# Kernel tuning notes

Hardware: AMD Instinct MI355X
Metric: run time of the kernel (lower is better)

Reference implementation:

```python
import jax, jax.numpy as jnp
import numpy as np

B, C, T = 8, 512, 2048
G = 32          # GroupNorm groups
HEADS = 8       # C // head_channels(64)
EPS = 1e-5


def setup_inputs() -> dict:
    key = jax.random.key(0)
    ks = jax.random.split(key, 7)
    s = 0.02
    return {
        "x": jax.random.normal(ks[0], (B, C, T), dtype=jnp.float32),
        "gn_w": jnp.ones((C,), dtype=jnp.float32),
        "gn_b": jnp.zeros((C,), dtype=jnp.float32),
        "qkv_w": jax.random.normal(ks[1], (3 * C, C), dtype=jnp.float32) * s,
        "qkv_b": jnp.zeros((3 * C,), dtype=jnp.float32),
        "proj_w": jax.random.normal(ks[2], (C, C), dtype=jnp.float32) * s,
        "proj_b": jnp.zeros((C,), dtype=jnp.float32),
    }


def reference(x, gn_w, gn_b, qkv_w, qkv_b, proj_w, proj_b):
    b, c, t = x.shape
    ch = c // HEADS
    # GroupNorm(32, C): normalize over (channels-in-group, T)
    xg = x.reshape(b, G, (c // G) * t)
    mu = jnp.mean(xg, axis=-1, keepdims=True)
    var = jnp.var(xg, axis=-1, keepdims=True)
    h = ((xg - mu) * jax.lax.rsqrt(var + EPS)).reshape(b, c, t)
    h = h * gn_w[:, None] + gn_b[:, None]
    # 1x1 Conv1d -> pointwise linear over channels
    qkv = jnp.einsum('oc,bct->bot', qkv_w, h) + qkv_b[:, None]  # [b, 3c, t]
    q, k, v = jnp.split(qkv, 3, axis=1)
    scale = ch ** -0.25
    q = (q * scale).reshape(b * HEADS, ch, t)
    k = (k * scale).reshape(b * HEADS, ch, t)
    v = v.reshape(b * HEADS, ch, t)
    w = jnp.einsum('bct,bcs->bts', q, k)  # [b*H, t, t]
    w = jax.nn.softmax(w.astype(jnp.float32), axis=-1).astype(q.dtype)
    a = jnp.einsum('bts,bcs->bct', w, v).reshape(b, c, t)
    out = jnp.einsum('oc,bct->bot', proj_w, a) + proj_b[:, None]
    return x + out
```

## Files before the change

kernel.cpp:

```cpp
#include <hip/hip_runtime.h>
#include <hip/hip_bf16.h>
#include <math.h>

#define NB 8
#define NC 512
#define NT 2048
#define NG 32
#define NH 8
#define CH 64

typedef __attribute__((ext_vector_type(8))) short short8;
typedef __attribute__((ext_vector_type(4))) short short4v;
typedef __attribute__((ext_vector_type(4))) float floatx4;

static __device__ __forceinline__ short f2bf(float f) {
    __hip_bfloat16 h = __float2bfloat16(f);
    return *reinterpret_cast<short*>(&h);
}

static __device__ __forceinline__ int pk2bf_trunc(float lo, float hi) {
    return (int)__builtin_amdgcn_perm(__builtin_bit_cast(unsigned, hi),
                                      __builtin_bit_cast(unsigned, lo),
                                      0x07060302u);
}

static __device__ __forceinline__ void gload_lds16(const short* g, short* l) {
    __builtin_amdgcn_global_load_lds(
        (const __attribute__((address_space(1))) void*)g,
        (__attribute__((address_space(3))) void*)l, 16, 0, 0);
}

__global__ __launch_bounds__(256) void castw_kernel(
    const float* __restrict__ w, short* __restrict__ o, int n4)
{
    const int i = blockIdx.x * 256 + threadIdx.x;
    if (i < n4) {
        float4 v = ((const float4*)w)[i];
        short4v s;
        s.x = f2bf(v.x); s.y = f2bf(v.y); s.z = f2bf(v.z); s.w = f2bf(v.w);
        *(short4v*)&o[i * 4] = s;
    }
}

__global__ __launch_bounds__(256) void gn_stats_kernel(
    const float* __restrict__ x, float* __restrict__ stats)
{
    __shared__ float red[16];
    const int tid = threadIdx.x;
    const int grp = blockIdx.x;
    const float4* xp = (const float4*)(x + (size_t)grp * 16 * NT);

    float s = 0.f, ss = 0.f;
    for (int i = tid; i < 8192; i += 256) {
        float4 v = xp[i];
        s  += v.x + v.y + v.z + v.w;
        ss += v.x*v.x + v.y*v.y + v.z*v.z + v.w*v.w;
    }
    #pragma unroll
    for (int o = 32; o > 0; o >>= 1) {
        s  += __shfl_down(s,  o, 64);
        ss += __shfl_down(ss, o, 64);
    }
    const int lane = tid & 63, wid = tid >> 6;
    if (lane == 0) { red[wid] = s; red[8 + wid] = ss; }
    __syncthreads();
    if (tid == 0) {
        const float inv = 1.f / 32768.f;
        const float mean = (red[0] + red[1] + red[2] + red[3]) * inv;
        const float var  = (red[8] + red[9] + red[10] + red[11]) * inv - mean * mean;
        stats[grp * 2]     = mean;
        stats[grp * 2 + 1] = rsqrtf(var + 1e-5f);
    }
}

__global__ __launch_bounds__(256) void gn_apply_kernel(
    const float* __restrict__ x, const float* __restrict__ gw,
    const float* __restrict__ gb, const float* __restrict__ stats,
    short* __restrict__ ht)
{
    __shared__ float wc_s[NC], bc_s[NC];
    const int tid = threadIdx.x;
    const int b = blockIdx.y;
    const int t0 = blockIdx.x * 64;

    for (int c = tid; c < NC; c += 256) {
        const int g = c >> 4;
        const float mean = stats[(b * NG + g) * 2];
        const float rstd = stats[(b * NG + g) * 2 + 1];
        const float wc = gw[c] * rstd;
        wc_s[c] = wc;
        bc_s[c] = gb[c] - mean * wc;
    }
    __syncthreads();

    const int t  = t0 + (tid >> 2);
    const int lc = tid & 3;
    const float* xb = x + (size_t)b * NC * NT + t;
    short* out = ht + ((size_t)b * NT + t) * NC;

    for (int k = 0; k < 16; ++k) {
        const int c0 = lc * 8 + k * 32;
        short8 v;
        #pragma unroll
        for (int j = 0; j < 8; ++j) {
            const int c = c0 + j;
            v[j] = f2bf(xb[(size_t)c * NT] * wc_s[c] + bc_s[c]);
        }
        *(short8*)&out[c0] = v;
    }
}

#define BK 32
__global__ __launch_bounds__(256) void qkv_gemm_kernel(
    const short* __restrict__ wb, const short* __restrict__ ht,
    const float* __restrict__ bias,
    short* __restrict__ q_t, short* __restrict__ k_t, short* __restrict__ vv)
{
    __shared__ short As[128 * BK];
    __shared__ short Bs[128 * BK];
    const int tid = threadIdx.x;
    const int wv = tid >> 6, lane = tid & 63;
    const int l16 = lane & 15, quad = lane >> 4;
    const int n0 = blockIdx.x * 128;
    const int m0 = blockIdx.y * 128;
    const int wm = wv & 1, wn = wv >> 1;

    floatx4 acc[4][4];
    #pragma unroll
    for (int i = 0; i < 4; ++i)
        #pragma unroll
        for (int j = 0; j < 4; ++j) acc[i][j] = (floatx4){0.f, 0.f, 0.f, 0.f};

    const short* gsrc = (wv < 2) ? wb : ht;
    const int rbase = (wv & 1) * 64;
    const int tile0 = (wv < 2) ? m0 : n0;
    short* lbuf = (wv < 2) ? As : Bs;
    const int lrow = lane >> 2;
    const int lcol = (lane & 3) * 8;

    for (int k0 = 0; k0 < 512; k0 += BK) {
        __syncthreads();
        #pragma unroll
        for (int ch = 0; ch < 4; ++ch) {
            const int row = rbase + ch * 16 + lrow;
            gload_lds16(gsrc + (size_t)(tile0 + row) * 512 + k0 + lcol,
                        lbuf + (rbase + ch * 16) * BK);
        }
        __syncthreads();

        short8 af[4], bfr[4];
        #pragma unroll
        for (int i = 0; i < 4; ++i) {
            af[i]  = *(const short8*)&As[(wm * 64 + i * 16 + l16) * BK + quad * 8];
            bfr[i] = *(const short8*)&Bs[(wn * 64 + i * 16 + l16) * BK + quad * 8];
        }
        #pragma unroll
        for (int i = 0; i < 4; ++i)
            #pragma unroll
            for (int j = 0; j < 4; ++j)
                acc[i][j] = __builtin_amdgcn_mfma_f32_16x16x32_bf16(
                    af[i], bfr[j], acc[i][j], 0, 0, 0);
    }

    const float kscale = 0.35355339059327373f;
    const float qscale = 0.35355339059327373f * 1.4426950408889634f;
    #pragma unroll
    for (int i = 0; i < 4; ++i) {
        const int o16 = m0 + wm * 64 + i * 16;
        const int sel = o16 >> 9;
        const int hh  = (o16 >> 6) & 7;
        const int c16 = o16 & 63;
        const float4 b4 = *(const float4*)&bias[o16 + quad * 4];
        const float sc = (sel == 0) ? qscale : kscale;
        #pragma unroll
        for (int j = 0; j < 4; ++j) {
            const int tg = n0 + wn * 64 + j * 16 + l16;
            const int b = tg >> 11, t = tg & 2047;
            floatx4 v = acc[i][j];
            v[0] += b4.x; v[1] += b4.y; v[2] += b4.z; v[3] += b4.w;
            if (sel < 2) {
                short4v s;
                s.x = f2bf(v[0] * sc); s.y = f2bf(v[1] * sc);
                s.z = f2bf(v[2] * sc); s.w = f2bf(v[3] * sc);
                short* dst = (sel == 0 ? q_t : k_t) +
                    (((size_t)(b * NH + hh) * NT + t) * CH + c16 + quad * 4);
                *(short4v*)dst = s;
            } else {
                short* dst = vv + ((size_t)(b * NH + hh) * CH + c16 + quad * 4) * NT + t;
                #pragma unroll
                for (int r = 0; r < 4; ++r) dst[(size_t)r * NT] = f2bf(v[r]);
            }
        }
    }
}

__global__ __launch_bounds__(256, 2) void attn_kernel(
    const short* __restrict__ qg, const short* __restrict__ kg,
    const short* __restrict__ vg, short* __restrict__ at)
{
    __shared__ short qps[256 * 64];
    __shared__ short kt[2][64 * 64];
    __shared__ short vs[2][64 * 64];

    const int tid = threadIdx.x;
    const int wv = tid >> 6, lane = tid & 63;
    const int l16 = lane & 15, quad = lane >> 4;
    const int xr = l16 & 7;
    const int t0 = blockIdx.x * 256;
    const int bh = blockIdx.y;
    const int b = bh >> 3, hd = bh & 7;
    const short* qh = qg + (size_t)bh * NT * CH;
    const short* kh = kg + (size_t)bh * NT * CH;
    const short* vh = vg + (size_t)bh * CH * NT;

    #pragma unroll
    for (int q = 0; q < 8; ++q) {
        const int F = (wv * 8 + q) * 64 + lane;
        const int row = F >> 3, cc = (F & 7) ^ (row & 7);
        gload_lds16(qh + (size_t)(t0 + row) * CH + cc * 8, &qps[(wv * 8 + q) * 512]);
    }
    #pragma unroll
    for (int q = 0; q < 2; ++q) {
        const int F = (wv * 2 + q) * 64 + lane;
        const int row = F >> 3, cc = (F & 7) ^ (row & 7);
        gload_lds16(kh + (size_t)row * CH + cc * 8, &kt[0][(wv * 2 + q) * 512]);
        gload_lds16(vh + (size_t)row * NT + cc * 8, &vs[0][(wv * 2 + q) * 512]);
    }
    __syncthreads();

    short8 bq[4][2];
    #pragma unroll
    for (int qt = 0; qt < 4; ++qt) {
        const int row = wv * 64 + qt * 16 + l16;
        #pragma unroll
        for (int ks = 0; ks < 2; ++ks) {
            const int c = (quad | (ks << 2)) ^ xr;
            bq[qt][ks] = *(const short8*)&qps[row * 64 + c * 8];
        }
    }

    floatx4 Oa[4][4];
    #pragma unroll
    for (int ct = 0; ct < 4; ++ct)
        #pragma unroll
        for (int qt = 0; qt < 4; ++qt) Oa[ct][qt] = (floatx4){0.f, 0.f, 0.f, 0.f};
    float l_part[4] = {0.f, 0.f, 0.f, 0.f};

    for (int it = 0; it < NT / 64; ++it) {
        __syncthreads();
        if (it + 1 < NT / 64) {
            const int s0n = (it + 1) * 64;
            short* kb = kt[(it + 1) & 1];
            short* vb = vs[(it + 1) & 1];
            #pragma unroll
            for (int q = 0; q < 2; ++q) {
                const int F = (wv * 2 + q) * 64 + lane;
                const int row = F >> 3, cc = (F & 7) ^ (row & 7);
                gload_lds16(kh + (size_t)(s0n + row) * CH + cc * 8, kb + (wv * 2 + q) * 512);
                gload_lds16(vh + (size_t)row * NT + s0n + cc * 8, vb + (wv * 2 + q) * 512);
            }
        }
        const short* kc = kt[it & 1];
        const short* vc = vs[it & 1];

        floatx4 sacc[4][4];
        #pragma unroll
        for (int nt = 0; nt < 4; ++nt)
            #pragma unroll
            for (int qt = 0; qt < 4; ++qt) sacc[nt][qt] = (floatx4){0.f, 0.f, 0.f, 0.f};
        #pragma unroll
        for (int ks = 0; ks < 2; ++ks) {
            const int c = (quad | (ks << 2)) ^ xr;
            #pragma unroll
            for (int nt = 0; nt < 4; ++nt) {
                short8 ak = *(const short8*)&kc[(nt * 16 + l16) * 64 + c * 8];
                #pragma unroll
                for (int qt = 0; qt < 4; ++qt)
                    sacc[nt][qt] = __builtin_amdgcn_mfma_f32_16x16x32_bf16(
                        ak, bq[qt][ks], sacc[nt][qt], 0, 0, 0);
            }
        }

        #pragma unroll
        for (int qt = 0; qt < 4; ++qt) {
            float sn[4];
            #pragma unroll
            for (int nt = 0; nt < 4; ++nt) {
                const float p0 = __builtin_amdgcn_exp2f(sacc[nt][qt][0]);
                const float p1 = __builtin_amdgcn_exp2f(sacc[nt][qt][1]);
                const float p2 = __builtin_amdgcn_exp2f(sacc[nt][qt][2]);
                const float p3 = __builtin_amdgcn_exp2f(sacc[nt][qt][3]);
                sacc[nt][qt][0] = p0; sacc[nt][qt][1] = p1;
                sacc[nt][qt][2] = p2; sacc[nt][qt][3] = p3;
                sn[nt] = (p0 + p1) + (p2 + p3);
            }
            l_part[qt] += (sn[0] + sn[1]) + (sn[2] + sn[3]);
        }

        #pragma unroll
        for (int qt = 0; qt < 4; ++qt) {
            const int row = wv * 64 + qt * 16 + l16;
            #pragma unroll
            for (int nt = 0; nt < 4; ++nt) {
                const int cw = (2 * nt + (quad >> 1)) ^ xr;
                int2 pv;
                pv.x = pk2bf_trunc(sacc[nt][qt][0], sacc[nt][qt][1]);
                pv.y = pk2bf_trunc(sacc[nt][qt][2], sacc[nt][qt][3]);
                *(int2*)&qps[row * 64 + cw * 8 + (quad & 1) * 4] = pv;
            }
        }

        #pragma unroll
        for (int ks = 0; ks < 2; ++ks) {
            const int c = (quad | (ks << 2)) ^ xr;
            short8 bp[4];
            #pragma unroll
            for (int qt = 0; qt < 4; ++qt)
                bp[qt] = *(const short8*)&qps[(wv * 64 + qt * 16 + l16) * 64 + c * 8];
            #pragma unroll
            for (int ct = 0; ct < 4; ++ct) {
                short8 av = *(const short8*)&vc[(ct * 16 + l16) * 64 + c * 8];
                #pragma unroll
                for (int qt = 0; qt < 4; ++qt)
                    Oa[ct][qt] = __builtin_amdgcn_mfma_f32_16x16x32_bf16(
                        av, bp[qt], Oa[ct][qt], 0, 0, 0);
            }
        }
    }

    #pragma unroll
    for (int qt = 0; qt < 4; ++qt) {
        float l = l_part[qt];
        l += __shfl_xor(l, 16, 64);
        l += __shfl_xor(l, 32, 64);
        const float rl = 1.f / l;
        const int t = t0 + wv * 64 + qt * 16 + l16;
        short* dst = at + ((size_t)b * NT + t) * NC + hd * CH;
        #pragma unroll
        for (int ct = 0; ct < 4; ++ct) {
            int2 s;
            s.x = pk2bf_trunc(Oa[ct][qt][0] * rl, Oa[ct][qt][1] * rl);
            s.y = pk2bf_trunc(Oa[ct][qt][2] * rl, Oa[ct][qt][3] * rl);
            *(int2*)&dst[ct * 16 + quad * 4] = s;
        }
    }
}

__global__ __launch_bounds__(256) void proj_gemm_kernel(
    const short* __restrict__ wb, const short* __restrict__ at,
    const float* __restrict__ bias, const float* __restrict__ xres,
    float* __restrict__ out)
{
    __shared__ short As[128 * BK];
    __shared__ short Bs[128 * BK];
    const int tid = threadIdx.x;
    const int wv = tid >> 6, lane = tid & 63;
    const int l16 = lane & 15, quad = lane >> 4;
    const int n0 = blockIdx.x * 128;
    const int m0 = blockIdx.y * 128;
    const int wm = wv & 1, wn = wv >> 1;

    floatx4 acc[4][4];
    #pragma unroll
    for (int i = 0; i < 4; ++i)
        #pragma unroll
        for (int j = 0; j < 4; ++j) acc[i][j] = (floatx4){0.f, 0.f, 0.f, 0.f};

    const short* gsrc = (wv < 2) ? wb : at;
    const int rbase = (wv & 1) * 64;
    const int tile0 = (wv < 2) ? m0 : n0;
    short* lbuf = (wv < 2) ? As : Bs;
    const int lrow = lane >> 2;
    const int lcol = (lane & 3) * 8;

    for (int k0 = 0; k0 < 512; k0 += BK) {
        __syncthreads();
        #pragma unroll
        for (int ch = 0; ch < 4; ++ch) {
            const int row = rbase + ch * 16 + lrow;
            gload_lds16(gsrc + (size_t)(tile0 + row) * 512 + k0 + lcol,
                        lbuf + (rbase + ch * 16) * BK);
        }
        __syncthreads();

        short8 af[4], bfr[4];
        #pragma unroll
        for (int i = 0; i < 4; ++i) {
            af[i]  = *(const short8*)&As[(wm * 64 + i * 16 + l16) * BK + quad * 8];
            bfr[i] = *(const short8*)&Bs[(wn * 64 + i * 16 + l16) * BK + quad * 8];
        }
        #pragma unroll
        for (int i = 0; i < 4; ++i)
            #pragma unroll
            for (int j = 0; j < 4; ++j)
                acc[i][j] = __builtin_amdgcn_mfma_f32_16x16x32_bf16(
                    af[i], bfr[j], acc[i][j], 0, 0, 0);
    }

    #pragma unroll
    for (int i = 0; i < 4; ++i) {
        const int o16 = m0 + wm * 64 + i * 16;
        const float4 b4 = *(const float4*)&bias[o16 + quad * 4];
        #pragma unroll
        for (int j = 0; j < 4; ++j) {
            const int tg = n0 + wn * 64 + j * 16 + l16;
            const int b = tg >> 11, t = tg & 2047;
            const size_t base = ((size_t)b * NC + o16 + quad * 4) * NT + t;
            floatx4 v = acc[i][j];
            out[base]          = v[0] + b4.x + xres[base];
            out[base + NT]     = v[1] + b4.y + xres[base + NT];
            out[base + 2 * NT] = v[2] + b4.z + xres[base + 2 * NT];
            out[base + 3 * NT] = v[3] + b4.w + xres[base + 3 * NT];
        }
    }
}

extern "C" void kernel_launch(void* const* d_in, const int* in_sizes, int n_in,
                              void* d_out, int out_size, void* d_ws, size_t ws_size,
                              hipStream_t stream)
{
    const float* x      = (const float*)d_in[0];
    const float* gn_w   = (const float*)d_in[1];
    const float* gn_b   = (const float*)d_in[2];
    const float* qkv_w  = (const float*)d_in[3];
    const float* qkv_b  = (const float*)d_in[4];
    const float* proj_w = (const float*)d_in[5];
    const float* proj_b = (const float*)d_in[6];
    float* out = (float*)d_out;

    short* ht  = (short*)d_ws;
    short* q_t = ht  + 8388608;
    short* k_t = q_t + 8388608;
    short* vv  = k_t + 8388608;
    short* at  = vv  + 8388608;
    short* qwb = at  + 8388608;
    short* pwb = qwb + 786432;
    float* stats = (float*)(pwb + 262144);

    castw_kernel<<<768, 256, 0, stream>>>(qkv_w, qwb, 1536 * 512 / 4);
    castw_kernel<<<256, 256, 0, stream>>>(proj_w, pwb, 512 * 512 / 4);
    gn_stats_kernel<<<NB * NG, 256, 0, stream>>>(x, stats);
    gn_apply_kernel<<<dim3(NT / 64, NB), 256, 0, stream>>>(x, gn_w, gn_b, stats, ht);
    qkv_gemm_kernel<<<dim3(128, 12), 256, 0, stream>>>(qwb, ht, qkv_b, q_t, k_t, vv);
    attn_kernel<<<dim3(NT / 256, NB * NH), 256, 0, stream>>>(q_t, k_t, vv, at);
    proj_gemm_kernel<<<dim3(128, 4), 256, 0, stream>>>(pwb, at, proj_b, x, out);
}
```

Measured before the change: 266.8 us.

## Widen attention blocks to 512 threads, transpose GN via LDS, merge weight casts

```diff
diff --git a/kernel.cpp b/kernel.cpp
--- a/kernel.cpp
+++ b/kernel.cpp
@@ -31,15 +31,17 @@
 }
 
 __global__ __launch_bounds__(256) void castw_kernel(
-    const float* __restrict__ w, short* __restrict__ o, int n4)
+    const float* __restrict__ qw, const float* __restrict__ pw,
+    short* __restrict__ qo, short* __restrict__ po)
 {
     const int i = blockIdx.x * 256 + threadIdx.x;
-    if (i < n4) {
-        float4 v = ((const float4*)w)[i];
-        short4v s;
-        s.x = f2bf(v.x); s.y = f2bf(v.y); s.z = f2bf(v.z); s.w = f2bf(v.w);
-        *(short4v*)&o[i * 4] = s;
-    }
+    const bool isq = i < 196608;
+    const int j = isq ? i : i - 196608;
+    float4 v = isq ? ((const float4*)qw)[j] : ((const float4*)pw)[j];
+    short4v s;
+    s.x = f2bf(v.x); s.y = f2bf(v.y); s.z = f2bf(v.z); s.w = f2bf(v.w);
+    if (isq) *(short4v*)&qo[j * 4] = s;
+    else     *(short4v*)&po[j * 4] = s;
 }
 
 __global__ __launch_bounds__(256) void gn_stats_kernel(
@@ -79,6 +81,7 @@
     short* __restrict__ ht)
 {
     __shared__ float wc_s[NC], bc_s[NC];
+    __shared__ float tile[64 * 68];
     const int tid = threadIdx.x;
     const int b = blockIdx.y;
     const int t0 = blockIdx.x * 64;
@@ -91,22 +94,31 @@
         wc_s[c] = wc;
         bc_s[c] = gb[c] - mean * wc;
     }
-    __syncthreads();
-
-    const int t  = t0 + (tid >> 2);
-    const int lc = tid & 3;
-    const float* xb = x + (size_t)b * NC * NT + t;
-    short* out = ht + ((size_t)b * NT + t) * NC;
-
-    for (int k = 0; k < 16; ++k) {
-        const int c0 = lc * 8 + k * 32;
-        short8 v;
-        #pragma unroll
-        for (int j = 0; j < 8; ++j) {
-            const int c = c0 + j;
-            v[j] = f2bf(xb[(size_t)c * NT] * wc_s[c] + bc_s[c]);
-        }
-        *(short8*)&out[c0] = v;
+
+    const int cl = tid >> 2;
+    const int k4 = tid & 3;
+    const int tl = tid >> 2;
+    const int cs = (tid & 3) * 16;
+
+    for (int p = 0; p < 8; ++p) {
+        const int c0 = p * 64;
+        __syncthreads();
+        const float* src = x + ((size_t)b * NC + c0 + cl) * NT + t0;
+        #pragma unroll
+        for (int k = 0; k < 4; ++k) {
+            float4 v = *(const float4*)(src + k4 * 16 + k * 4);
+            *(float4*)&tile[cl * 68 + k4 * 16 + k * 4] = v;
+        }
+        __syncthreads();
+        short v16[16];
+        #pragma unroll
+        for (int j = 0; j < 16; ++j) {
+            const int c = c0 + cs + j;
+            v16[j] = f2bf(tile[(cs + j) * 68 + tl] * wc_s[c] + bc_s[c]);
+        }
+        short* dst = ht + ((size_t)b * NT + t0 + tl) * NC + c0 + cs;
+        *(short8*)&dst[0] = *(const short8*)&v16[0];
+        *(short8*)&dst[8] = *(const short8*)&v16[8];
     }
 }
 
@@ -194,7 +206,7 @@
     }
 }
 
-__global__ __launch_bounds__(256, 2) void attn_kernel(
+__global__ __launch_bounds__(512, 4) void attn_kernel(
     const short* __restrict__ qg, const short* __restrict__ kg,
     const short* __restrict__ vg, short* __restrict__ at)
 {
@@ -214,24 +226,22 @@
     const short* vh = vg + (size_t)bh * CH * NT;
 
     #pragma unroll
-    for (int q = 0; q < 8; ++q) {
-        const int F = (wv * 8 + q) * 64 + lane;
+    for (int q = 0; q < 4; ++q) {
+        const int F = (wv * 4 + q) * 64 + lane;
         const int row = F >> 3, cc = (F & 7) ^ (row & 7);
-        gload_lds16(qh + (size_t)(t0 + row) * CH + cc * 8, &qps[(wv * 8 + q) * 512]);
-    }
-    #pragma unroll
-    for (int q = 0; q < 2; ++q) {
-        const int F = (wv * 2 + q) * 64 + lane;
-        const int row = F >> 3, cc = (F & 7) ^ (row & 7);
-        gload_lds16(kh + (size_t)row * CH + cc * 8, &kt[0][(wv * 2 + q) * 512]);
-        gload_lds16(vh + (size_t)row * NT + cc * 8, &vs[0][(wv * 2 + q) * 512]);
+        gload_lds16(qh + (size_t)(t0 + row) * CH + cc * 8, &qps[(wv * 4 + q) * 512]);
+    }
+    {
+        const int row = tid >> 3, cc = (tid & 7) ^ (row & 7);
+        gload_lds16(kh + (size_t)row * CH + cc * 8, &kt[0][wv * 512]);
+        gload_lds16(vh + (size_t)row * NT + cc * 8, &vs[0][wv * 512]);
     }
     __syncthreads();
 
-    short8 bq[4][2];
-    #pragma unroll
-    for (int qt = 0; qt < 4; ++qt) {
-        const int row = wv * 64 + qt * 16 + l16;
+    short8 bq[2][2];
+    #pragma unroll
+    for (int qt = 0; qt < 2; ++qt) {
+        const int row = wv * 32 + qt * 16 + l16;
         #pragma unroll
         for (int ks = 0; ks < 2; ++ks) {
             const int c = (quad | (ks << 2)) ^ xr;
@@ -239,35 +249,31 @@
         }
     }
 
-    floatx4 Oa[4][4];
+    floatx4 Oa[4][2];
     #pragma unroll
     for (int ct = 0; ct < 4; ++ct)
         #pragma unroll
-        for (int qt = 0; qt < 4; ++qt) Oa[ct][qt] = (floatx4){0.f, 0.f, 0.f, 0.f};
-    float l_part[4] = {0.f, 0.f, 0.f, 0.f};
+        for (int qt = 0; qt < 2; ++qt) Oa[ct][qt] = (floatx4){0.f, 0.f, 0.f, 0.f};
+    float l_part[2] = {0.f, 0.f};
 
     for (int it = 0; it < NT / 64; ++it) {
         __syncthreads();
         if (it + 1 < NT / 64) {
             const int s0n = (it + 1) * 64;
-            short* kb = kt[(it + 1) & 1];
-            short* vb = vs[(it + 1) & 1];
-            #pragma unroll
-            for (int q = 0; q < 2; ++q) {
-                const int F = (wv * 2 + q) * 64 + lane;
-                const int row = F >> 3, cc = (F & 7) ^ (row & 7);
-                gload_lds16(kh + (size_t)(s0n + row) * CH + cc * 8, kb + (wv * 2 + q) * 512);
-                gload_lds16(vh + (size_t)row * NT + s0n + cc * 8, vb + (wv * 2 + q) * 512);
-            }
+            const int row = tid >> 3, cc = (tid & 7) ^ (row & 7);
+            gload_lds16(kh + (size_t)(s0n + row) * CH + cc * 8,
+                        &kt[(it + 1) & 1][wv * 512]);
+            gload_lds16(vh + (size_t)row * NT + s0n + cc * 8,
+                        &vs[(it + 1) & 1][wv * 512]);
         }
         const short* kc = kt[it & 1];
         const short* vc = vs[it & 1];
 
-        floatx4 sacc[4][4];
+        floatx4 sacc[4][2];
         #pragma unroll
         for (int nt = 0; nt < 4; ++nt)
             #pragma unroll
-            for (int qt = 0; qt < 4; ++qt) sacc[nt][qt] = (floatx4){0.f, 0.f, 0.f, 0.f};
+            for (int qt = 0; qt < 2; ++qt) sacc[nt][qt] = (floatx4){0.f, 0.f, 0.f, 0.f};
         #pragma unroll
         for (int ks = 0; ks < 2; ++ks) {
             const int c = (quad | (ks << 2)) ^ xr;
@@ -275,14 +281,14 @@
             for (int nt = 0; nt < 4; ++nt) {
                 short8 ak = *(const short8*)&kc[(nt * 16 + l16) * 64 + c * 8];
                 #pragma unroll
-                for (int qt = 0; qt < 4; ++qt)
+                for (int qt = 0; qt < 2; ++qt)
                     sacc[nt][qt] = __builtin_amdgcn_mfma_f32_16x16x32_bf16(
                         ak, bq[qt][ks], sacc[nt][qt], 0, 0, 0);
             }
         }
 
         #pragma unroll
-        for (int qt = 0; qt < 4; ++qt) {
+        for (int qt = 0; qt < 2; ++qt) {
             float sn[4];
             #pragma unroll
             for (int nt = 0; nt < 4; ++nt) {
@@ -298,8 +304,8 @@
         }
 
         #pragma unroll
-        for (int qt = 0; qt < 4; ++qt) {
-            const int row = wv * 64 + qt * 16 + l16;
+        for (int qt = 0; qt < 2; ++qt) {
+            const int row = wv * 32 + qt * 16 + l16;
             #pragma unroll
             for (int nt = 0; nt < 4; ++nt) {
                 const int cw = (2 * nt + (quad >> 1)) ^ xr;
@@ -313,15 +319,15 @@
         #pragma unroll
         for (int ks = 0; ks < 2; ++ks) {
             const int c = (quad | (ks << 2)) ^ xr;
-            short8 bp[4];
-            #pragma unroll
-            for (int qt = 0; qt < 4; ++qt)
-                bp[qt] = *(const short8*)&qps[(wv * 64 + qt * 16 + l16) * 64 + c * 8];
+            short8 bp[2];
+            #pragma unroll
+            for (int qt = 0; qt < 2; ++qt)
+                bp[qt] = *(const short8*)&qps[(wv * 32 + qt * 16 + l16) * 64 + c * 8];
             #pragma unroll
             for (int ct = 0; ct < 4; ++ct) {
                 short8 av = *(const short8*)&vc[(ct * 16 + l16) * 64 + c * 8];
                 #pragma unroll
-                for (int qt = 0; qt < 4; ++qt)
+                for (int qt = 0; qt < 2; ++qt)
                     Oa[ct][qt] = __builtin_amdgcn_mfma_f32_16x16x32_bf16(
                         av, bp[qt], Oa[ct][qt], 0, 0, 0);
             }
@@ -329,12 +335,12 @@
     }
 
     #pragma unroll
-    for (int qt = 0; qt < 4; ++qt) {
+    for (int qt = 0; qt < 2; ++qt) {
         float l = l_part[qt];
         l += __shfl_xor(l, 16, 64);
         l += __shfl_xor(l, 32, 64);
         const float rl = 1.f / l;
-        const int t = t0 + wv * 64 + qt * 16 + l16;
+        const int t = t0 + wv * 32 + qt * 16 + l16;
         short* dst = at + ((size_t)b * NT + t) * NC + hd * CH;
         #pragma unroll
         for (int ct = 0; ct < 4; ++ct) {
@@ -437,11 +443,10 @@
     short* pwb = qwb + 786432;
     float* stats = (float*)(pwb + 262144);
 
-    castw_kernel<<<768, 256, 0, stream>>>(qkv_w, qwb, 1536 * 512 / 4);
-    castw_kernel<<<256, 256, 0, stream>>>(proj_w, pwb, 512 * 512 / 4);
+    castw_kernel<<<1024, 256, 0, stream>>>(qkv_w, proj_w, qwb, pwb);
     gn_stats_kernel<<<NB * NG, 256, 0, stream>>>(x, stats);
     gn_apply_kernel<<<dim3(NT / 64, NB), 256, 0, stream>>>(x, gn_w, gn_b, stats, ht);
     qkv_gemm_kernel<<<dim3(128, 12), 256, 0, stream>>>(qwb, ht, qkv_b, q_t, k_t, vv);
-    attn_kernel<<<dim3(NT / 256, NB * NH), 256, 0, stream>>>(q_t, k_t, vv, at);
+    attn_kernel<<<dim3(NT / 256, NB * NH), 512, 0, stream>>>(q_t, k_t, vv, at);
     proj_gemm_kernel<<<dim3(128, 4), 256, 0, stream>>>(pwb, at, proj_b, x, out);
 }
```

Measured after the change: 264.1 us. Within noise of the previous version (-1.0%).
